# Optimization experiments

Hardware: AMD Instinct MI355X
Metric: run time of the kernel (lower is better)

## Reference

```python
import jax, jax.numpy as jnp
import numpy as np

EPS = 1e-08
TEMPERATURE = 1.0
HEADS = 4
OUT_DIM = 32
IN_DIM = 128
N_NODES = 100000
N_EDGES = 1600000


def setup_inputs() -> dict:
    key = jax.random.key(0)
    k1, k2, k3, k4, k5, k6 = jax.random.split(key, 6)
    x = jax.random.normal(k1, (N_NODES, IN_DIM), dtype=jnp.float32)
    # nn.Linear(in_dim, heads*out_dim, bias=False).weight -> [heads*out_dim, in_dim]
    W = jax.random.normal(k2, (HEADS * OUT_DIM, IN_DIM), dtype=jnp.float32) * 0.05
    a_src = jax.random.normal(k3, (HEADS, OUT_DIM), dtype=jnp.float32) * 0.1
    a_dst = jax.random.normal(k4, (HEADS, OUT_DIM), dtype=jnp.float32) * 0.1
    edge_index = jax.random.randint(k5, (2, N_EDGES), 0, N_NODES, dtype=jnp.int32)
    rnbrw_weights = jax.random.uniform(k6, (N_EDGES,), dtype=jnp.float32)
    return {"x": x, "W": W, "a_src": a_src, "a_dst": a_dst,
            "edge_index": edge_index, "rnbrw_weights": rnbrw_weights}


def reference(x, W, a_src, a_dst, edge_index, rnbrw_weights):
    N = x.shape[0]
    heads, out_dim = a_src.shape
    # h = W(x).view(N, heads, out_dim)
    h = (x @ W.T).reshape(N, heads, out_dim)
    src, dst = edge_index[0], edge_index[1]
    h_src = h[src]  # [E, heads, out_dim]
    h_dst = h[dst]  # [E, heads, out_dim]
    # per-edge attention scores [E, heads]
    score = jnp.einsum('ehd,hd->eh', h_src, a_src) + jnp.einsum('ehd,hd->eh', h_dst, a_dst)
    # strategy == 'pre_softmax_bias'
    score = score + jnp.log(rnbrw_weights + EPS)[:, None]
    score = jnp.where(score >= 0, score, 0.2 * score)  # leaky_relu(0.2)
    scaled = score / TEMPERATURE
    # edge softmax over incoming edges of each dst node
    seg_max = jax.ops.segment_max(scaled, dst, num_segments=N)      # [N, heads]
    exp_s = jnp.exp(scaled - seg_max[dst])                           # [E, heads]
    denom = jax.ops.segment_sum(exp_s, dst, num_segments=N)         # [N, heads]
    alpha = exp_s / (denom[dst] + EPS)                               # [E, heads]
    # scatter-add aggregation: out[dst] += alpha * h_src
    out = jax.ops.segment_sum(alpha[..., None] * h_src, dst, num_segments=N)
    out = out.reshape(N, heads * out_dim)
    return out, alpha
```

## Files before the change

kernel.cpp:

```cpp
#include <hip/hip_runtime.h>

#define EPS 1e-8f

__device__ inline unsigned short f2bf(float f) {
    unsigned u = __float_as_uint(f);
    unsigned r = u + 0x7fffu + ((u >> 16) & 1u);
    return (unsigned short)(r >> 16);
}
__device__ inline float bflo(unsigned v) { return __uint_as_float(v << 16); }
__device__ inline float bfhi(unsigned v) { return __uint_as_float(v & 0xffff0000u); }

__global__ __launch_bounds__(256) void gemm_s_kernel(
    const float* __restrict__ x, const float* __restrict__ W,
    const float* __restrict__ a_src, const float* __restrict__ a_dst,
    unsigned short* __restrict__ hb, float* __restrict__ s_src, float* __restrict__ s_dst,
    int N, int n_tiles)
{
    __shared__ float Wt[128 * 64];
    __shared__ float xt[128 * 64];

    const int t = threadIdx.x;
    const int half = blockIdx.y;
    const float* Wh = W + half * 64 * 128;

#pragma unroll
    for (int p = 0; p < 8; ++p) {
        int idx = p * 256 + t;
        int ol = (idx & 31) | ((idx >> 10) << 5);
        int k4 = (idx >> 5) & 31;
        float4 w = *(const float4*)(Wh + ol * 128 + k4 * 4);
        Wt[(4 * k4 + 0) * 64 + ol] = w.x;
        Wt[(4 * k4 + 1) * 64 + ol] = w.y;
        Wt[(4 * k4 + 2) * 64 + ol] = w.z;
        Wt[(4 * k4 + 3) * 64 + ol] = w.w;
    }
    __syncthreads();

    const int o4 = t & 15;
    const int n4g = t >> 4;
    const int head = half * 2 + (o4 >> 3);
    const float4 as = *(const float4*)(a_src + head * 32 + (o4 & 7) * 4);
    const float4 ad = *(const float4*)(a_dst + head * 32 + (o4 & 7) * 4);

    for (int tile = blockIdx.x; tile < n_tiles; tile += gridDim.x) {
        const int nbase = tile * 64;
        __syncthreads();
#pragma unroll
        for (int p = 0; p < 8; ++p) {
            int idx = p * 256 + t;
            int n = idx & 63;
            int k4 = idx >> 6;
            int ng = nbase + n;
            float4 v = make_float4(0.f, 0.f, 0.f, 0.f);
            if (ng < N) v = *(const float4*)(x + (size_t)ng * 128 + k4 * 4);
            xt[(4 * k4 + 0) * 64 + n] = v.x;
            xt[(4 * k4 + 1) * 64 + n] = v.y;
            xt[(4 * k4 + 2) * 64 + n] = v.z;
            xt[(4 * k4 + 3) * 64 + n] = v.w;
        }
        __syncthreads();

        float acc[4][4];
#pragma unroll
        for (int i = 0; i < 4; ++i)
#pragma unroll
            for (int j = 0; j < 4; ++j) acc[i][j] = 0.f;

        for (int k = 0; k < 128; ++k) {
            float4 wv = *(const float4*)(Wt + k * 64 + 4 * o4);
            float4 xv = *(const float4*)(xt + k * 64 + 4 * n4g);
            float wa[4] = {wv.x, wv.y, wv.z, wv.w};
            float xa[4] = {xv.x, xv.y, xv.z, xv.w};
#pragma unroll
            for (int i = 0; i < 4; ++i)
#pragma unroll
                for (int j = 0; j < 4; ++j) acc[i][j] += xa[i] * wa[j];
        }

#pragma unroll
        for (int i = 0; i < 4; ++i) {
            int n = nbase + 4 * n4g + i;
            float ps = acc[i][0] * as.x + acc[i][1] * as.y + acc[i][2] * as.z + acc[i][3] * as.w;
            float pd = acc[i][0] * ad.x + acc[i][1] * ad.y + acc[i][2] * ad.z + acc[i][3] * ad.w;
            ps += __shfl_xor(ps, 1); ps += __shfl_xor(ps, 2); ps += __shfl_xor(ps, 4);
            pd += __shfl_xor(pd, 1); pd += __shfl_xor(pd, 2); pd += __shfl_xor(pd, 4);
            if (n < N) {
                ushort4 hv;
                hv.x = f2bf(acc[i][0]); hv.y = f2bf(acc[i][1]);
                hv.z = f2bf(acc[i][2]); hv.w = f2bf(acc[i][3]);
                *(ushort4*)(hb + (size_t)n * 128 + half * 64 + 4 * o4) = hv;
                if ((o4 & 7) == 0) {
                    s_src[n * 4 + head] = ps;
                    s_dst[n * 4 + head] = pd;
                }
            }
        }
    }
}

__global__ __launch_bounds__(256) void count_kernel(
    const int* __restrict__ dst, int* __restrict__ counts, int E)
{
    int e = blockIdx.x * 256 + threadIdx.x;
    if (e < E) atomicAdd(counts + dst[e], 1);
}

__global__ __launch_bounds__(256) void scan1_kernel(
    const int* __restrict__ counts, int* __restrict__ offs, int* __restrict__ bsum, int N)
{
    __shared__ int sh[256];
    int t = threadIdx.x;
    int base = blockIdx.x * 1024 + t * 4;
    int c[4];
#pragma unroll
    for (int j = 0; j < 4; ++j) c[j] = (base + j < N) ? counts[base + j] : 0;
    int tsum = c[0] + c[1] + c[2] + c[3];
    sh[t] = tsum;
    __syncthreads();
    for (int off = 1; off < 256; off <<= 1) {
        int v = (t >= off) ? sh[t - off] : 0;
        __syncthreads();
        sh[t] += v;
        __syncthreads();
    }
    int run = sh[t] - tsum;
    if (t == 255) bsum[blockIdx.x] = sh[255];
#pragma unroll
    for (int j = 0; j < 4; ++j) {
        if (base + j < N) { offs[base + j] = run; run += c[j]; }
    }
}

__global__ void scan2_kernel(int* __restrict__ bsum, int nb)
{
    if (threadIdx.x == 0) {
        int acc = 0;
        for (int i = 0; i < nb; ++i) { int v = bsum[i]; bsum[i] = acc; acc += v; }
    }
}

__global__ __launch_bounds__(256) void scan3_kernel(
    int* __restrict__ offs, const int* __restrict__ bsum,
    int* __restrict__ cursor, int N)
{
    int i = blockIdx.x * 256 + threadIdx.x;
    if (i >= N) return;
    int v = offs[i] + bsum[i >> 10];
    offs[i] = v;
    cursor[i] = v;
}

__global__ __launch_bounds__(256) void scatter_kernel(
    const int* __restrict__ src, const int* __restrict__ dst,
    const float* __restrict__ rnbrw,
    int* __restrict__ cursor, int2* __restrict__ rec,
    int E, int ssz, int bps)
{
    const int shard = blockIdx.x & 7;
    const int j = blockIdx.x >> 3;
    const int lo = shard * ssz;
    const int hi = lo + ssz;
    const int stride = bps * 256;
    for (int base = j * 256; base < E; base += stride) {
        int e = base + threadIdx.x;
        if (e < E) {
            int d = dst[e];
            if (d >= lo && d < hi) {
                float lw = __logf(rnbrw[e] + EPS);
                int pos = atomicAdd(cursor + d, 1);
                rec[pos] = make_int2(src[e], __float_as_int(lw));
            }
        }
    }
}

__global__ __launch_bounds__(256) void node_aggr_kernel(
    const int* __restrict__ offs, const int* __restrict__ counts,
    const int2* __restrict__ rec,
    const float* __restrict__ s_src, const float* __restrict__ s_dst,
    const unsigned short* __restrict__ hb,
    float* __restrict__ inv_den, float* __restrict__ out, int N)
{
    int gid = blockIdx.x * 256 + threadIdx.x;
    int n = gid >> 5;
    int l = gid & 31;
    if (n >= N) return;

    const int q    = l & 15;
    const int half = l >> 4;
    const int head = q >> 2;

    const int beg = offs[n];
    const int cnt = counts[n];
    const float sdn = s_dst[n * 4 + head];

    float a0 = 0.f, a1 = 0.f, a2 = 0.f, a3 = 0.f;
    float a4 = 0.f, a5 = 0.f, a6 = 0.f, a7 = 0.f;
    float den = 0.f;

    for (int i = 0; i < cnt; i += 4) {
        int j0 = i + half;
        int j1 = i + 2 + half;
        int jc0 = (j0 < cnt) ? j0 : 0;
        int jc1 = (j1 < cnt) ? j1 : 0;
        int2 r0 = rec[(size_t)beg + jc0];
        int2 r1 = rec[(size_t)beg + jc1];
        uint4 v0 = *(const uint4*)(hb + (size_t)r0.x * 128 + q * 8);
        uint4 v1 = *(const uint4*)(hb + (size_t)r1.x * 128 + q * 8);
        float t0 = s_src[(size_t)r0.x * 4 + head] + sdn + __int_as_float(r0.y);
        float t1 = s_src[(size_t)r1.x * 4 + head] + sdn + __int_as_float(r1.y);
        t0 = (t0 >= 0.f) ? t0 : 0.2f * t0;
        t1 = (t1 >= 0.f) ? t1 : 0.2f * t1;
        float e0 = __expf(t0);
        float e1 = __expf(t1);
        if (j0 >= cnt) e0 = 0.f;
        if (j1 >= cnt) e1 = 0.f;
        a0 += e0 * bflo(v0.x); a1 += e0 * bfhi(v0.x);
        a2 += e0 * bflo(v0.y); a3 += e0 * bfhi(v0.y);
        a4 += e0 * bflo(v0.z); a5 += e0 * bfhi(v0.z);
        a6 += e0 * bflo(v0.w); a7 += e0 * bfhi(v0.w);
        a0 += e1 * bflo(v1.x); a1 += e1 * bfhi(v1.x);
        a2 += e1 * bflo(v1.y); a3 += e1 * bfhi(v1.y);
        a4 += e1 * bflo(v1.z); a5 += e1 * bfhi(v1.z);
        a6 += e1 * bflo(v1.w); a7 += e1 * bfhi(v1.w);
        den += e0 + e1;
    }

    a0 += __shfl_xor(a0, 16, 32); a1 += __shfl_xor(a1, 16, 32);
    a2 += __shfl_xor(a2, 16, 32); a3 += __shfl_xor(a3, 16, 32);
    a4 += __shfl_xor(a4, 16, 32); a5 += __shfl_xor(a5, 16, 32);
    a6 += __shfl_xor(a6, 16, 32); a7 += __shfl_xor(a7, 16, 32);
    den += __shfl_xor(den, 16, 32);

    const float inv = 1.f / (den + EPS);

    float d0 = __shfl(den, 0, 32);
    float d1 = __shfl(den, 4, 32);
    float d2 = __shfl(den, 8, 32);
    float d3 = __shfl(den, 12, 32);

    float4 o = half ? make_float4(a4 * inv, a5 * inv, a6 * inv, a7 * inv)
                    : make_float4(a0 * inv, a1 * inv, a2 * inv, a3 * inv);
    *(float4*)(out + (size_t)n * 128 + q * 8 + half * 4) = o;

    if (l == 0)
        *(float4*)(inv_den + (size_t)n * 4) =
            make_float4(1.f / (d0 + EPS), 1.f / (d1 + EPS),
                        1.f / (d2 + EPS), 1.f / (d3 + EPS));
}

__global__ __launch_bounds__(256) void alpha_kernel(
    const int* __restrict__ src, const int* __restrict__ dst,
    const float* __restrict__ rnbrw,
    const float* __restrict__ s_src, const float* __restrict__ s_dst,
    const float* __restrict__ inv_den, float* __restrict__ alpha, int E)
{
    int e = blockIdx.x * 256 + threadIdx.x;
    if (e >= E) return;
    int s = src[e], d = dst[e];
    float lw = __logf(rnbrw[e] + EPS);
    float4 a = *(const float4*)(s_src + s * 4);
    float4 b = *(const float4*)(s_dst + d * 4);
    float4 iv = *(const float4*)(inv_den + (size_t)d * 4);
    float4 al;
    float v;
    v = a.x + b.x + lw; v = (v >= 0.f) ? v : 0.2f * v; al.x = __expf(v) * iv.x;
    v = a.y + b.y + lw; v = (v >= 0.f) ? v : 0.2f * v; al.y = __expf(v) * iv.y;
    v = a.z + b.z + lw; v = (v >= 0.f) ? v : 0.2f * v; al.z = __expf(v) * iv.z;
    v = a.w + b.w + lw; v = (v >= 0.f) ? v : 0.2f * v; al.w = __expf(v) * iv.w;
    *(float4*)(alpha + (size_t)e * 4) = al;
}

extern "C" void kernel_launch(void* const* d_in, const int* in_sizes, int n_in,
                              void* d_out, int out_size, void* d_ws, size_t ws_size,
                              hipStream_t stream) {
    const float* x      = (const float*)d_in[0];
    const float* W      = (const float*)d_in[1];
    const float* a_src  = (const float*)d_in[2];
    const float* a_dst  = (const float*)d_in[3];
    const int*   eidx   = (const int*)d_in[4];
    const float* rnbrw  = (const float*)d_in[5];

    const int E = in_sizes[5];
    const int N = in_sizes[0] / 128;

    float* out   = (float*)d_out;
    float* alpha = out + (size_t)N * 128;

    char* w = (char*)d_ws;
    unsigned short* hb = (unsigned short*)w;  w += (size_t)N * 128 * 2;
    int2* rec     = (int2*)w;                 w += (size_t)E * 8;
    float* s_src  = (float*)w;                w += (size_t)N * 16;
    float* s_dst  = (float*)w;                w += (size_t)N * 16;
    float* inv_den = (float*)w;               w += (size_t)N * 16;
    int* counts  = (int*)w;                   w += (size_t)N * 4;
    int* offs    = (int*)w;                   w += (size_t)N * 4;
    int* cursor  = (int*)w;                   w += (size_t)N * 4;
    int* bsum    = (int*)w;                   w += 512;

    const int* src = eidx;
    const int* dst = eidx + E;

    hipMemsetAsync(counts, 0, (size_t)N * sizeof(int), stream);

    int eblocks = (E + 255) / 256;
    count_kernel<<<eblocks, 256, 0, stream>>>(dst, counts, E);

    int n_tiles = (N + 63) / 64;
    dim3 gridA(512, 2);
    gemm_s_kernel<<<gridA, 256, 0, stream>>>(x, W, a_src, a_dst, hb, s_src, s_dst, N, n_tiles);

    int nb = (N + 1023) / 1024;
    scan1_kernel<<<nb, 256, 0, stream>>>(counts, offs, bsum, N);
    scan2_kernel<<<1, 64, 0, stream>>>(bsum, nb);
    scan3_kernel<<<(N + 255) / 256, 256, 0, stream>>>(offs, bsum, cursor, N);

    int ssz = (N + 7) / 8;
    int bps = 256;
    scatter_kernel<<<8 * bps, 256, 0, stream>>>(src, dst, rnbrw, cursor, rec, E, ssz, bps);

    int ablocks = ((size_t)N * 32 + 255) / 256;
    node_aggr_kernel<<<ablocks, 256, 0, stream>>>(offs, counts, rec, s_src, s_dst, hb,
                                                  inv_den, out, N);

    alpha_kernel<<<eblocks, 256, 0, stream>>>(src, dst, rnbrw, s_src, s_dst,
                                              inv_den, alpha, E);
}
```

Baseline: 433.1 us.

## Fuse GEMM and edge scatter into one heterogeneous kernel launch

Merges the projection GEMM and the CSR scatter into a single launch. One third of the blocks do the GEMM tiles and two thirds do the sharded edge scatter, with block roles interleaved by group index so compute-bound and atomic/memory-bound work share the GPU at the same time. The x tile in shared memory is cut to a 32-wide K chunk so occupancy can rise (launch bounds 256,4). The cost is more syncthreads per tile and a fixed 3072-block layout that assumes 1024 GEMM blocks.

```diff
diff --git a/kernel.cpp b/kernel.cpp
--- a/kernel.cpp
+++ b/kernel.cpp
@@ -9,94 +9,6 @@
 }
 __device__ inline float bflo(unsigned v) { return __uint_as_float(v << 16); }
 __device__ inline float bfhi(unsigned v) { return __uint_as_float(v & 0xffff0000u); }
-
-__global__ __launch_bounds__(256) void gemm_s_kernel(
-    const float* __restrict__ x, const float* __restrict__ W,
-    const float* __restrict__ a_src, const float* __restrict__ a_dst,
-    unsigned short* __restrict__ hb, float* __restrict__ s_src, float* __restrict__ s_dst,
-    int N, int n_tiles)
-{
-    __shared__ float Wt[128 * 64];
-    __shared__ float xt[128 * 64];
-
-    const int t = threadIdx.x;
-    const int half = blockIdx.y;
-    const float* Wh = W + half * 64 * 128;
-
-#pragma unroll
-    for (int p = 0; p < 8; ++p) {
-        int idx = p * 256 + t;
-        int ol = (idx & 31) | ((idx >> 10) << 5);
-        int k4 = (idx >> 5) & 31;
-        float4 w = *(const float4*)(Wh + ol * 128 + k4 * 4);
-        Wt[(4 * k4 + 0) * 64 + ol] = w.x;
-        Wt[(4 * k4 + 1) * 64 + ol] = w.y;
-        Wt[(4 * k4 + 2) * 64 + ol] = w.z;
-        Wt[(4 * k4 + 3) * 64 + ol] = w.w;
-    }
-    __syncthreads();
-
-    const int o4 = t & 15;
-    const int n4g = t >> 4;
-    const int head = half * 2 + (o4 >> 3);
-    const float4 as = *(const float4*)(a_src + head * 32 + (o4 & 7) * 4);
-    const float4 ad = *(const float4*)(a_dst + head * 32 + (o4 & 7) * 4);
-
-    for (int tile = blockIdx.x; tile < n_tiles; tile += gridDim.x) {
-        const int nbase = tile * 64;
-        __syncthreads();
-#pragma unroll
-        for (int p = 0; p < 8; ++p) {
-            int idx = p * 256 + t;
-            int n = idx & 63;
-            int k4 = idx >> 6;
-            int ng = nbase + n;
-            float4 v = make_float4(0.f, 0.f, 0.f, 0.f);
-            if (ng < N) v = *(const float4*)(x + (size_t)ng * 128 + k4 * 4);
-            xt[(4 * k4 + 0) * 64 + n] = v.x;
-            xt[(4 * k4 + 1) * 64 + n] = v.y;
-            xt[(4 * k4 + 2) * 64 + n] = v.z;
-            xt[(4 * k4 + 3) * 64 + n] = v.w;
-        }
-        __syncthreads();
-
-        float acc[4][4];
-#pragma unroll
-        for (int i = 0; i < 4; ++i)
-#pragma unroll
-            for (int j = 0; j < 4; ++j) acc[i][j] = 0.f;
-
-        for (int k = 0; k < 128; ++k) {
-            float4 wv = *(const float4*)(Wt + k * 64 + 4 * o4);
-            float4 xv = *(const float4*)(xt + k * 64 + 4 * n4g);
-            float wa[4] = {wv.x, wv.y, wv.z, wv.w};
-            float xa[4] = {xv.x, xv.y, xv.z, xv.w};
-#pragma unroll
-            for (int i = 0; i < 4; ++i)
-#pragma unroll
-                for (int j = 0; j < 4; ++j) acc[i][j] += xa[i] * wa[j];
-        }
-
-#pragma unroll
-        for (int i = 0; i < 4; ++i) {
-            int n = nbase + 4 * n4g + i;
-            float ps = acc[i][0] * as.x + acc[i][1] * as.y + acc[i][2] * as.z + acc[i][3] * as.w;
-            float pd = acc[i][0] * ad.x + acc[i][1] * ad.y + acc[i][2] * ad.z + acc[i][3] * ad.w;
-            ps += __shfl_xor(ps, 1); ps += __shfl_xor(ps, 2); ps += __shfl_xor(ps, 4);
-            pd += __shfl_xor(pd, 1); pd += __shfl_xor(pd, 2); pd += __shfl_xor(pd, 4);
-            if (n < N) {
-                ushort4 hv;
-                hv.x = f2bf(acc[i][0]); hv.y = f2bf(acc[i][1]);
-                hv.z = f2bf(acc[i][2]); hv.w = f2bf(acc[i][3]);
-                *(ushort4*)(hb + (size_t)n * 128 + half * 64 + 4 * o4) = hv;
-                if ((o4 & 7) == 0) {
-                    s_src[n * 4 + head] = ps;
-                    s_dst[n * 4 + head] = pd;
-                }
-            }
-        }
-    }
-}
 
 __global__ __launch_bounds__(256) void count_kernel(
     const int* __restrict__ dst, int* __restrict__ counts, int E)
@@ -150,25 +62,118 @@
     cursor[i] = v;
 }
 
-__global__ __launch_bounds__(256) void scatter_kernel(
+__global__ __launch_bounds__(256, 4) void fused_gemm_scatter_kernel(
+    const float* __restrict__ x, const float* __restrict__ W,
+    const float* __restrict__ a_src, const float* __restrict__ a_dst,
+    unsigned short* __restrict__ hb, float* __restrict__ s_src, float* __restrict__ s_dst,
+    int N, int n_tiles,
     const int* __restrict__ src, const int* __restrict__ dst,
     const float* __restrict__ rnbrw,
-    int* __restrict__ cursor, int2* __restrict__ rec,
-    int E, int ssz, int bps)
-{
-    const int shard = blockIdx.x & 7;
-    const int j = blockIdx.x >> 3;
-    const int lo = shard * ssz;
-    const int hi = lo + ssz;
-    const int stride = bps * 256;
-    for (int base = j * 256; base < E; base += stride) {
-        int e = base + threadIdx.x;
-        if (e < E) {
-            int d = dst[e];
-            if (d >= lo && d < hi) {
-                float lw = __logf(rnbrw[e] + EPS);
-                int pos = atomicAdd(cursor + d, 1);
-                rec[pos] = make_int2(src[e], __float_as_int(lw));
+    int* __restrict__ cursor, int2* __restrict__ rec, int E, int ssz)
+{
+    __shared__ float Wt[128 * 64];
+    __shared__ float xt[32 * 64];
+
+    const int bid  = blockIdx.x;
+    const int grp  = bid >> 3;
+    const int l7   = bid & 7;
+
+    if (grp % 3 == 0) {
+        const int g    = (grp / 3) * 8 + l7;
+        const int half = g >> 9;
+        const int bx   = g & 511;
+        const int t    = threadIdx.x;
+        const float* Wh = W + half * 64 * 128;
+
+#pragma unroll
+        for (int p = 0; p < 8; ++p) {
+            int idx = p * 256 + t;
+            int ol = (idx & 31) | ((idx >> 10) << 5);
+            int k4 = (idx >> 5) & 31;
+            float4 w = *(const float4*)(Wh + ol * 128 + k4 * 4);
+            Wt[(4 * k4 + 0) * 64 + ol] = w.x;
+            Wt[(4 * k4 + 1) * 64 + ol] = w.y;
+            Wt[(4 * k4 + 2) * 64 + ol] = w.z;
+            Wt[(4 * k4 + 3) * 64 + ol] = w.w;
+        }
+        __syncthreads();
+
+        const int o4 = t & 15;
+        const int n4g = t >> 4;
+        const int head = half * 2 + (o4 >> 3);
+        const float4 as = *(const float4*)(a_src + head * 32 + (o4 & 7) * 4);
+        const float4 ad = *(const float4*)(a_dst + head * 32 + (o4 & 7) * 4);
+
+        for (int tile = bx; tile < n_tiles; tile += 512) {
+            const int nbase = tile * 64;
+
+            float acc[4][4];
+#pragma unroll
+            for (int i = 0; i < 4; ++i)
+#pragma unroll
+                for (int j = 0; j < 4; ++j) acc[i][j] = 0.f;
+
+            for (int kc = 0; kc < 4; ++kc) {
+                __syncthreads();
+#pragma unroll
+                for (int p = 0; p < 2; ++p) {
+                    int idx = p * 256 + t;
+                    int n = idx & 63;
+                    int k4 = idx >> 6;
+                    int ng = nbase + n;
+                    float4 v = make_float4(0.f, 0.f, 0.f, 0.f);
+                    if (ng < N) v = *(const float4*)(x + (size_t)ng * 128 + kc * 32 + k4 * 4);
+                    xt[(4 * k4 + 0) * 64 + n] = v.x;
+                    xt[(4 * k4 + 1) * 64 + n] = v.y;
+                    xt[(4 * k4 + 2) * 64 + n] = v.z;
+                    xt[(4 * k4 + 3) * 64 + n] = v.w;
+                }
+                __syncthreads();
+
+                for (int k = 0; k < 32; ++k) {
+                    float4 wv = *(const float4*)(Wt + (kc * 32 + k) * 64 + 4 * o4);
+                    float4 xv = *(const float4*)(xt + k * 64 + 4 * n4g);
+                    float wa[4] = {wv.x, wv.y, wv.z, wv.w};
+                    float xa[4] = {xv.x, xv.y, xv.z, xv.w};
+#pragma unroll
+                    for (int i = 0; i < 4; ++i)
+#pragma unroll
+                        for (int j = 0; j < 4; ++j) acc[i][j] += xa[i] * wa[j];
+                }
+            }
+
+#pragma unroll
+            for (int i = 0; i < 4; ++i) {
+                int n = nbase + 4 * n4g + i;
+                float ps = acc[i][0] * as.x + acc[i][1] * as.y + acc[i][2] * as.z + acc[i][3] * as.w;
+                float pd = acc[i][0] * ad.x + acc[i][1] * ad.y + acc[i][2] * ad.z + acc[i][3] * ad.w;
+                ps += __shfl_xor(ps, 1); ps += __shfl_xor(ps, 2); ps += __shfl_xor(ps, 4);
+                pd += __shfl_xor(pd, 1); pd += __shfl_xor(pd, 2); pd += __shfl_xor(pd, 4);
+                if (n < N) {
+                    ushort4 hv;
+                    hv.x = f2bf(acc[i][0]); hv.y = f2bf(acc[i][1]);
+                    hv.z = f2bf(acc[i][2]); hv.w = f2bf(acc[i][3]);
+                    *(ushort4*)(hb + (size_t)n * 128 + half * 64 + 4 * o4) = hv;
+                    if ((o4 & 7) == 0) {
+                        s_src[n * 4 + head] = ps;
+                        s_dst[n * 4 + head] = pd;
+                    }
+                }
+            }
+        }
+    } else {
+        const int j  = grp - grp / 3 - 1;
+        const int lo = l7 * ssz;
+        const int hi = lo + ssz;
+        for (int base = j * 256; base < E; base += 256 * 256) {
+            int e = base + threadIdx.x;
+            if (e < E) {
+                int d = dst[e];
+                if (d >= lo && d < hi) {
+                    float lw = __logf(rnbrw[e] + EPS);
+                    int pos = atomicAdd(cursor + d, 1);
+                    rec[pos] = make_int2(src[e], __float_as_int(lw));
+                }
             }
         }
     }
@@ -306,18 +311,16 @@
     int eblocks = (E + 255) / 256;
     count_kernel<<<eblocks, 256, 0, stream>>>(dst, counts, E);
 
-    int n_tiles = (N + 63) / 64;
-    dim3 gridA(512, 2);
-    gemm_s_kernel<<<gridA, 256, 0, stream>>>(x, W, a_src, a_dst, hb, s_src, s_dst, N, n_tiles);
-
     int nb = (N + 1023) / 1024;
     scan1_kernel<<<nb, 256, 0, stream>>>(counts, offs, bsum, N);
     scan2_kernel<<<1, 64, 0, stream>>>(bsum, nb);
     scan3_kernel<<<(N + 255) / 256, 256, 0, stream>>>(offs, bsum, cursor, N);
 
+    int n_tiles = (N + 63) / 64;
     int ssz = (N + 7) / 8;
-    int bps = 256;
-    scatter_kernel<<<8 * bps, 256, 0, stream>>>(src, dst, rnbrw, cursor, rec, E, ssz, bps);
+    fused_gemm_scatter_kernel<<<3072, 256, 0, stream>>>(
+        x, W, a_src, a_dst, hb, s_src, s_dst, N, n_tiles,
+        src, dst, rnbrw, cursor, rec, E, ssz);
 
     int ablocks = ((size_t)N * 32 + 255) / 256;
     node_aggr_kernel<<<ablocks, 256, 0, stream>>>(offs, counts, rec, s_src, s_dst, hb,
```

Result: slower. 457.7 us (+5.7%).
